# Kernel optimization log

Measured on AMD Instinct MI355X. Metric: run time of the kernel, lower is better.

## Reference

```python
import jax, jax.numpy as jnp
import numpy as np

DIM = 768; HEADS = 12; N_PH = 4; EXPERTS = 8; TOPK = 2; EXPERT_DIM = 3072; MEM_HEADS = 8; EPS = 1e-5


def phm_linear(x, A, S, b):
    # PHM linear: W = sum_i kron(A[i] (n,n), S[i] (out/n, in/n)) -> (out, in); y = x @ W.T + b
    out_f = A.shape[1] * S.shape[1]
    in_f = A.shape[2] * S.shape[2]
    W = jnp.einsum('iab,icd->acbd', A, S).reshape(out_f, in_f)
    return x @ W.T + b


def layernorm(x, g, b):
    m = x.mean(-1, keepdims=True)
    v = x.var(-1, keepdims=True)
    return (x - m) / jnp.sqrt(v + EPS) * g + b


def quantum_attn(x, A_qkv, S_qkv, b_qkv, A_p, S_p, b_p, w_sup, w_ent):
    B, N, C = x.shape
    hd = C // HEADS
    qkv = phm_linear(x, A_qkv, S_qkv, b_qkv).reshape(B, N, 3, HEADS, hd)
    qkv = qkv.transpose(2, 0, 3, 1, 4)  # (3,B,H,N,hd)
    q, k, v = qkv[0], qkv[1], qkv[2]
    attn = jnp.einsum('bhnd,bhmd->bhnm', q, k) * (hd ** -0.5)
    # superposition head-mixing: sup[:,i] = sum_j w_sup[i,j] * attn[:,j]
    sup = jnp.einsum('ij,bjnm->binm', w_sup, attn)
    # entanglement: ent[:,i] = tanh(sup[:,i] + sum_j w_ent[i,j] * sup[:,j])
    ent = jnp.tanh(sup + jnp.einsum('ij,bjnm->binm', w_ent, sup))
    a = jax.nn.softmax(ent, axis=-1)
    o = jnp.einsum('bhnm,bhmd->bnhd', a, v).reshape(B, N, C)
    return phm_linear(o, A_p, S_p, b_p)


def moe(x, rA, rS, rb, domain_routing, domain_id, eA, eS, eb, ndw, ndb):
    logits = phm_linear(x, rA, rS, rb) + domain_routing[domain_id]  # (B,N,E)
    topv, topi = jax.lax.top_k(logits, TOPK)
    w = jax.nn.softmax(topv, axis=-1)  # (B,N,K)
    onehot = (topi[..., None] == jnp.arange(EXPERTS)).astype(x.dtype)  # (B,N,K,E)
    gates = jnp.einsum('bnk,bnke->bne', w, onehot)  # combined top-k gate per expert

    def expert(Ae, Se, be, We, bne):
        h = jax.nn.gelu(phm_linear(x, Ae, Se, be), approximate=False)
        return h @ We.T + bne

    outs = jax.vmap(expert)(eA, eS, eb, ndw, ndb)  # (E,B,N,C)
    return jnp.einsum('bne,ebnc->bnc', gates, outs)


def mem_mha(x, mem, iw, ib, ow, ob):
    # standard MHA: queries from x (B,N,C), keys/values from memory bank (M,C) shared across batch
    B, N, C = x.shape
    dh = C // MEM_HEADS
    q = (x @ iw[:C].T + ib[:C]).reshape(B, N, MEM_HEADS, dh)
    k = (mem @ iw[C:2 * C].T + ib[C:2 * C]).reshape(-1, MEM_HEADS, dh)
    v = (mem @ iw[2 * C:].T + ib[2 * C:]).reshape(-1, MEM_HEADS, dh)
    a = jax.nn.softmax(jnp.einsum('bnhd,mhd->bhnm', q, k) * (dh ** -0.5), axis=-1)
    o = jnp.einsum('bhnm,mhd->bnhd', a, v).reshape(B, N, C)
    return o @ ow.T + ob


def fractal(x, mems, iw, ib, ow, ob, pw, pb):
    # recursive FractalMemoryBank unrolled for depth=3:
    # level l: a_l = proc_l(MHA_l(prev, mem_l)); return prev + deeper(a_l)
    a0 = mem_mha(x, mems[0], iw[0], ib[0], ow[0], ob[0]) @ pw[0].T + pb[0]
    a1 = mem_mha(a0, mems[1], iw[1], ib[1], ow[1], ob[1]) @ pw[1].T + pb[1]
    a2 = mem_mha(a1, mems[2], iw[2], ib[2], ow[2], ob[2]) @ pw[2].T + pb[2]
    return x + (a0 + (a1 + a2))


def _fwd(x, ln1_g, ln1_b, attn_qkv_A, attn_qkv_S, attn_qkv_b, attn_proj_A, attn_proj_S, attn_proj_b,
         w_sup, w_ent, ln2_g, ln2_b, router_A, router_S, router_b, domain_routing,
         exp_A, exp_S, exp_b, exp_nd_w, exp_nd_b, mem0, mem1, mem2,
         mha_in_w, mha_in_b, mha_out_w, mha_out_b, proc_w, proc_b, ln3_g, ln3_b, domain_id):
    attended = x + quantum_attn(layernorm(x, ln1_g, ln1_b), attn_qkv_A, attn_qkv_S, attn_qkv_b,
                                attn_proj_A, attn_proj_S, attn_proj_b, w_sup, w_ent)
    moe_out = moe(layernorm(attended, ln2_g, ln2_b), router_A, router_S, router_b,
                  domain_routing, domain_id, exp_A, exp_S, exp_b, exp_nd_w, exp_nd_b)
    eo = attended + moe_out
    mo = fractal(eo, (mem0, mem1, mem2), mha_in_w, mha_in_b, mha_out_w, mha_out_b, proc_w, proc_b)
    return layernorm(mo, ln3_g, ln3_b)


def setup_inputs():
    key = jax.random.key(0)
    ks = iter(jax.random.split(key, 40))

    def rn(shape, s=0.02):
        return s * jax.random.normal(next(ks), shape, dtype=jnp.float32)

    B, N = 4, 512
    ones = jnp.ones(DIM, jnp.float32)
    zeros = jnp.zeros(DIM, jnp.float32)
    return {
        'x': rn((B, N, DIM), 1.0),
        'ln1_g': ones, 'ln1_b': zeros, 'ln2_g': ones, 'ln2_b': zeros, 'ln3_g': ones, 'ln3_b': zeros,
        'attn_qkv_A': rn((N_PH, N_PH, N_PH), 0.3),
        'attn_qkv_S': rn((N_PH, 3 * DIM // N_PH, DIM // N_PH)),
        'attn_qkv_b': jnp.zeros(3 * DIM, jnp.float32),
        'attn_proj_A': rn((N_PH, N_PH, N_PH), 0.3),
        'attn_proj_S': rn((N_PH, DIM // N_PH, DIM // N_PH)),
        'attn_proj_b': zeros,
        'w_sup': rn((HEADS, HEADS), 0.2), 'w_ent': rn((HEADS, HEADS), 0.2),
        'router_A': rn((N_PH, N_PH, N_PH), 0.3),
        'router_S': rn((N_PH, EXPERTS // N_PH, DIM // N_PH)),
        'router_b': jnp.zeros(EXPERTS, jnp.float32),
        'domain_routing': rn((6, EXPERTS), 1.0),
        'exp_A': rn((EXPERTS, N_PH, N_PH, N_PH), 0.3),
        'exp_S': rn((EXPERTS, N_PH, EXPERT_DIM // N_PH, DIM // N_PH)),
        'exp_b': jnp.zeros((EXPERTS, EXPERT_DIM), jnp.float32),
        'exp_nd_w': rn((EXPERTS, DIM, EXPERT_DIM)),
        'exp_nd_b': jnp.zeros((EXPERTS, DIM), jnp.float32),
        'mem0': rn((64, DIM), 1.0), 'mem1': rn((128, DIM), 1.0), 'mem2': rn((256, DIM), 1.0),
        'mha_in_w': rn((3, 3 * DIM, DIM)), 'mha_in_b': jnp.zeros((3, 3 * DIM), jnp.float32),
        'mha_out_w': rn((3, DIM, DIM)), 'mha_out_b': jnp.zeros((3, DIM), jnp.float32),
        'proc_w': rn((3, DIM, DIM)), 'proc_b': jnp.zeros((3, DIM), jnp.float32),
        'domain_id': 2,
    }


def reference(x, ln1_g, ln1_b, ln2_g, ln2_b, ln3_g, ln3_b, attn_qkv_A, attn_qkv_S, attn_qkv_b,
              attn_proj_A, attn_proj_S, attn_proj_b, w_sup, w_ent, router_A, router_S, router_b,
              domain_routing, exp_A, exp_S, exp_b, exp_nd_w, exp_nd_b, mem0, mem1, mem2,
              mha_in_w, mha_in_b, mha_out_w, mha_out_b, proc_w, proc_b, domain_id):
    return _fwd(x, ln1_g, ln1_b, attn_qkv_A, attn_qkv_S, attn_qkv_b, attn_proj_A, attn_proj_S,
                attn_proj_b, w_sup, w_ent, ln2_g, ln2_b, router_A, router_S, router_b,
                domain_routing, exp_A, exp_S, exp_b, exp_nd_w, exp_nd_b, mem0, mem1, mem2,
                mha_in_w, mha_in_b, mha_out_w, mha_out_b, proc_w, proc_b, ln3_g, ln3_b, domain_id)
```

## Files before the change

kernel.cpp:

```cpp
#include <hip/hip_runtime.h>
#include <math.h>

#define DIM    768
#define NTOK   2048
#define NSEQ   512
#define NBATCH 4
#define NHEADS 12
#define HD     64
#define QKVC   2304
#define MHEADS 8
#define MHD    96
#define NEXP   8
#define EDIM   3072
#define DD     (DIM*DIM)

typedef unsigned short u16;
typedef __attribute__((ext_vector_type(8))) short short8;
typedef __attribute__((ext_vector_type(4))) float f32x4;

struct L3 { long a, b, c; };
struct I3 { int a, b, c; };
struct CJ { const float4* s[6]; ushort4* d[6]; int n4[6]; };

__device__ __forceinline__ float gelu_exact(float v){
    return 0.5f * v * (1.f + erff(v * 0.70710678118654752f));
}
__device__ __forceinline__ u16 f2bf(float f){
    unsigned int u = __builtin_bit_cast(unsigned int, f);
    unsigned int r = (u + 0x7FFFu + ((u >> 16) & 1u)) >> 16;
    return (u16)r;
}
__device__ __forceinline__ float bf2f(u16 b){
    unsigned int u = ((unsigned int)b) << 16;
    return __builtin_bit_cast(float, u);
}
__device__ __forceinline__ float fast_tanh(float s){
    return 1.f - 2.f/(__expf(2.f*s) + 1.f);
}
__device__ __forceinline__ void gll16(const u16* g, u16* l){
    __builtin_amdgcn_global_load_lds((const __attribute__((address_space(1))) void*)g,
                                     (__attribute__((address_space(3))) void*)l, 16, 0, 0);
}

template<int WM,int WN,int FR,int DB>
__device__ __forceinline__ void mgemm_core(
    const u16* __restrict__ Xb, int ldx, int rowBase, int rowLim,
    const u16* __restrict__ Wb, int ldw, int colBase, int colLim, int K,
    const float* __restrict__ bias,
    const float* __restrict__ res, int ldres,
    float* __restrict__ Cf, u16* __restrict__ Cb, int ldc,
    float scale, int act)
{
    constexpr int TM = 16*FR;
    constexpr int RM = WM*TM, RN = WN*TM, NT = WM*WN*64;
    constexpr int IA = (RM*8)/NT, IB = (RN*8)/NT;
    constexpr int NB = DB ? 2 : 1;
    __shared__ u16 As[NB][RM*64];
    __shared__ u16 Bs[NB][RN*64];
    int tid = threadIdx.x;
    int lane = tid & 63, w = tid >> 6;
    int wm = (w / WN) * TM, wn = (w % WN) * TM;
    const f32x4 zf = {0.f, 0.f, 0.f, 0.f};
    f32x4 acc[FR][FR];
    #pragma unroll
    for (int i=0;i<FR;i++)
        #pragma unroll
        for (int j=0;j<FR;j++) acc[i][j] = zf;

    const bool fullA = (rowBase + RM <= rowLim);
    const bool fullB = (colBase + RN <= colLim);
    const int nt = (K + 63) >> 6;
    int lr = lane & 15, lk = lane >> 4;

    auto stage = [&](int buf, int k0){
        const bool kfull = (k0 + 64 <= K);
        if (fullA && kfull) {
            #pragma unroll
            for (int it = 0; it < IA; ++it) {
                int idx = it*NT + tid;
                int r = idx >> 3, c = idx & 7;
                gll16(&Xb[(size_t)(rowBase + r)*ldx + k0 + ((c ^ (r & 7)) << 3)], &As[buf][(size_t)idx*8]);
            }
        } else {
            #pragma unroll
            for (int it = 0; it < IA; ++it) {
                int idx = it*NT + tid;
                int r = idx >> 3, c = idx & 7;
                int gr = rowBase + r;
                uint4 v = {0u,0u,0u,0u};
                if (gr < rowLim && (k0 + c*8) < K) v = *(const uint4*)&Xb[(size_t)gr*ldx + k0 + c*8];
                *(uint4*)&As[buf][r*64 + ((c ^ (r & 7)) * 8)] = v;
            }
        }
        if (fullB && kfull) {
            #pragma unroll
            for (int it = 0; it < IB; ++it) {
                int idx = it*NT + tid;
                int r = idx >> 3, c = idx & 7;
                gll16(&Wb[(size_t)(colBase + r)*ldw + k0 + ((c ^ (r & 7)) << 3)], &Bs[buf][(size_t)idx*8]);
            }
        } else {
            #pragma unroll
            for (int it = 0; it < IB; ++it) {
                int idx = it*NT + tid;
                int r = idx >> 3, c = idx & 7;
                int gc = colBase + r;
                uint4 v = {0u,0u,0u,0u};
                if (gc < colLim && (k0 + c*8) < K) v = *(const uint4*)&Wb[(size_t)gc*ldw + k0 + c*8];
                *(uint4*)&Bs[buf][r*64 + ((c ^ (r & 7)) * 8)] = v;
            }
        }
    };
    auto compute = [&](const u16* Ac, const u16* Bc){
        #pragma unroll
        for (int ks = 0; ks < 2; ++ks) {
            short8 af[FR], bfr[FR];
            #pragma unroll
            for (int mi=0; mi<FR; mi++){
                int row = wm + mi*16 + lr;
                int cidx = (ks*4 + lk) ^ (row & 7);
                af[mi] = *(const short8*)&Ac[row*64 + cidx*8];
            }
            #pragma unroll
            for (int ni=0; ni<FR; ni++){
                int col = wn + ni*16 + lr;
                int cidx = (ks*4 + lk) ^ (col & 7);
                bfr[ni] = *(const short8*)&Bc[col*64 + cidx*8];
            }
            #pragma unroll
            for (int mi=0; mi<FR; mi++)
                #pragma unroll
                for (int ni=0; ni<FR; ni++)
                    acc[mi][ni] = __builtin_amdgcn_mfma_f32_16x16x32_bf16(af[mi], bfr[ni], acc[mi][ni], 0, 0, 0);
        }
    };

    if (DB) {
        stage(0, 0);
        __syncthreads();
        for (int t = 0; t < nt; ++t) {
            if (t + 1 < nt) stage((t+1)&1, (t+1)*64);
            compute(As[t&1], Bs[t&1]);
            __syncthreads();
        }
    } else {
        for (int t = 0; t < nt; ++t) {
            stage(0, t*64);
            __syncthreads();
            compute(As[0], Bs[0]);
            __syncthreads();
        }
    }
    int lg = lane >> 4;
    #pragma unroll
    for (int mi=0; mi<FR; mi++){
        #pragma unroll
        for (int r=0; r<4; r++){
            int row = rowBase + wm + mi*16 + lg*4 + r;
            if (row >= rowLim) continue;
            #pragma unroll
            for (int ni=0; ni<FR; ni++){
                int col = colBase + wn + ni*16 + lr;
                if (col >= colLim) continue;
                float v = acc[mi][ni][r] * scale;
                if (bias) v += bias[col];
                if (act == 1) v = gelu_exact(v);
                if (Cb) Cb[(size_t)row*ldc + col] = f2bf(v);
                if (res) v += res[(size_t)row*ldres + col];
                if (Cf) Cf[(size_t)row*ldc + col] = v;
            }
        }
    }
}

template<int WM,int WN,int FR,int DB>
__global__ __launch_bounds__(WM*WN*64) void k_mgemm(
    const u16* __restrict__ X, int ldx, int M,
    const u16* __restrict__ W, int ldw, int N, int K,
    const float* __restrict__ bias, const float* __restrict__ res, int ldres,
    float* __restrict__ Cf, u16* __restrict__ Cb, int ldc, float scale, int act)
{
    constexpr int RM = WM*16*FR, RN = WN*16*FR;
    mgemm_core<WM,WN,FR,DB>(X, ldx, blockIdx.x*RM, M, W, ldw, blockIdx.y*RN, N, K,
                            bias, res, ldres, Cf, Cb, ldc, scale, act);
}

template<int WM,int WN,int FR,int DB>
__global__ __launch_bounds__(WM*WN*64) void k_mgemm_b3(
    const u16* __restrict__ X, L3 xo, int ldx, I3 Mv,
    const u16* __restrict__ W, L3 wo, int ldw, int N, int K,
    const float* __restrict__ bias, L3 bo,
    u16* __restrict__ Cb, L3 co, int ldc, float scale, int act)
{
    constexpr int RM = WM*16*FR, RN = WN*16*FR;
    int z = blockIdx.z;
    int M    = (z==0) ? Mv.a : (z==1) ? Mv.b : Mv.c;
    long xof = (z==0) ? xo.a : (z==1) ? xo.b : xo.c;
    long wof = (z==0) ? wo.a : (z==1) ? wo.b : wo.c;
    long bof = (z==0) ? bo.a : (z==1) ? bo.b : bo.c;
    long cof = (z==0) ? co.a : (z==1) ? co.b : co.c;
    if ((int)blockIdx.x * RM >= M) return;
    mgemm_core<WM,WN,FR,DB>(X + xof, ldx, blockIdx.x*RM, M, W + wof, ldw, blockIdx.y*RN, N, K,
                            bias ? bias + bof : nullptr, nullptr, 0, nullptr, Cb + cof, ldc, scale, act);
}

template<int WM,int WN,int FR,int DB>
__global__ __launch_bounds__(WM*WN*64) void k_mgemm_expert(
    const u16* __restrict__ X, int ldx,
    const u16* __restrict__ Wb, int ldw, long wStride,
    const float* __restrict__ biasB, int biasStride,
    const int* __restrict__ prefix, const int* __restrict__ cnt,
    float* __restrict__ Cf, u16* __restrict__ Cb, int ldc, int N, int K, int act)
{
    constexpr int RM = WM*16*FR, RN = WN*16*FR;
    int e = blockIdx.z;
    int n = cnt[e];
    if ((int)blockIdx.x * RM >= n) return;
    mgemm_core<WM,WN,FR,DB>(X, ldx, prefix[e] + blockIdx.x*RM, prefix[e] + n,
                            Wb + (size_t)e*wStride, ldw, blockIdx.y*RN, N, K,
                            biasB + (size_t)e*biasStride, nullptr, 0, Cf, Cb, ldc, 1.f, act);
}

template<int WM,int WN,int FR,int DB>
__global__ __launch_bounds__(WM*WN*64) void k_mgemm_qk(const u16* __restrict__ qkv, u16* __restrict__ attn)
{
    constexpr int RM = WM*16*FR, RN = WN*16*FR;
    int z = blockIdx.z, b = z / NHEADS, h = z % NHEADS;
    const u16* X = qkv + (size_t)b*NSEQ*QKVC + h*HD;
    const u16* W = qkv + (size_t)b*NSEQ*QKVC + DIM + h*HD;
    u16* C = attn + (size_t)z*NSEQ*NSEQ;
    mgemm_core<WM,WN,FR,DB>(X, QKVC, blockIdx.x*RM, NSEQ, W, QKVC, blockIdx.y*RN, NSEQ, HD,
                            nullptr, nullptr, 0, nullptr, C, NSEQ, 0.125f, 0);
}

template<int WM,int WN,int FR,int DB>
__global__ __launch_bounds__(WM*WN*64) void k_mgemm_pv(const u16* __restrict__ P, const u16* __restrict__ Vt, u16* __restrict__ o)
{
    constexpr int RM = WM*16*FR, RN = WN*16*FR;
    int z = blockIdx.z, b = z / NHEADS, h = z % NHEADS;
    const u16* X = P + (size_t)z*NSEQ*NSEQ;
    const u16* W = Vt + ((size_t)b*DIM + h*HD)*NSEQ;
    u16* C = o + (size_t)b*NSEQ*DIM + h*HD;
    mgemm_core<WM,WN,FR,DB>(X, NSEQ, blockIdx.x*RM, NSEQ, W, NSEQ, blockIdx.y*RN, HD, NSEQ,
                            nullptr, nullptr, 0, nullptr, C, DIM, 1.f, 0);
}

template<int WM,int WN,int FR,int DB>
__global__ __launch_bounds__(WM*WN*64) void k_gt(
    const u16* __restrict__ Wc, const u16* __restrict__ kvL, long kvStride,
    u16* __restrict__ Gt, long gtStride, I3 Mv)
{
    constexpr int RM = WM*16*FR, RN = WN*16*FR;
    int z = blockIdx.z, l = z >> 3, h = z & 7;
    int M = (l==0) ? Mv.a : (l==1) ? Mv.b : Mv.c;
    if ((int)blockIdx.y * RN >= M) return;
    mgemm_core<WM,WN,FR,DB>(Wc + (size_t)l*DD + h*MHD, DIM, blockIdx.x*RM, DIM,
                            kvL + (size_t)l*kvStride + DIM + h*MHD, 2*DIM, blockIdx.y*RN, M, MHD,
                            nullptr, nullptr, 0, nullptr,
                            Gt + (size_t)l*gtStride + (size_t)h*M, 8*M, 1.f, 0);
}

__global__ __launch_bounds__(256) void k_memqk_soft(
    const u16* __restrict__ q, const u16* __restrict__ kv, int ldk,
    u16* __restrict__ P, int M, float scale)
{
    constexpr int RM = 64, RN = 256, NT = 256, K = MHD;
    __shared__ u16 As[RM*64];
    __shared__ u16 Bs[RN*64];
    __shared__ float red0[RM][4];
    __shared__ float red1[RM][4];
    int h = blockIdx.y;
    int rowBase = blockIdx.x * RM;
    const u16* Xb = q + h*MHD;
    const u16* Wb = kv + h*MHD;
    int tid = threadIdx.x, lane = tid & 63, w = tid >> 6;
    int wn = w * 64;
    int lr = lane & 15, lk = lane >> 4;
    const f32x4 zf = {0.f,0.f,0.f,0.f};
    f32x4 acc[4][4];
    #pragma unroll
    for (int i=0;i<4;i++)
        #pragma unroll
        for (int j=0;j<4;j++) acc[i][j] = zf;

    for (int k0 = 0; k0 < K; k0 += 64) {
        const bool kfull = (k0 + 64 <= K);
        if (kfull) {
            #pragma unroll
            for (int it = 0; it < 2; ++it) {
                int idx = it*NT + tid;
                int r = idx >> 3, c = idx & 7;
                gll16(&Xb[(size_t)(rowBase + r)*DIM + k0 + ((c ^ (r & 7)) << 3)], &As[(size_t)idx*8]);
            }
        } else {
            #pragma unroll
            for (int it = 0; it < 2; ++it) {
                int idx = it*NT + tid;
                int r = idx >> 3, c = idx & 7;
                uint4 v = {0u,0u,0u,0u};
                if ((k0 + c*8) < K) v = *(const uint4*)&Xb[(size_t)(rowBase + r)*DIM + k0 + c*8];
                *(uint4*)&As[r*64 + ((c ^ (r & 7)) * 8)] = v;
            }
        }
        #pragma unroll
        for (int it = 0; it < 8; ++it) {
            int idx = it*NT + tid;
            int r = idx >> 3, c = idx & 7;
            uint4 v = {0u,0u,0u,0u};
            if (r < M && (k0 + c*8) < K) v = *(const uint4*)&Wb[(size_t)r*ldk + k0 + c*8];
            *(uint4*)&Bs[r*64 + ((c ^ (r & 7)) * 8)] = v;
        }
        __syncthreads();
        #pragma unroll
        for (int ks = 0; ks < 2; ++ks) {
            short8 af[4], bfr[4];
            #pragma unroll
            for (int mi=0; mi<4; mi++){
                int row = mi*16 + lr;
                int cidx = (ks*4 + lk) ^ (row & 7);
                af[mi] = *(const short8*)&As[row*64 + cidx*8];
            }
            #pragma unroll
            for (int ni=0; ni<4; ni++){
                int col = wn + ni*16 + lr;
                int cidx = (ks*4 + lk) ^ (col & 7);
                bfr[ni] = *(const short8*)&Bs[col*64 + cidx*8];
            }
            #pragma unroll
            for (int mi=0; mi<4; mi++)
                #pragma unroll
                for (int ni=0; ni<4; ni++)
                    acc[mi][ni] = __builtin_amdgcn_mfma_f32_16x16x32_bf16(af[mi], bfr[ni], acc[mi][ni], 0, 0, 0);
        }
        __syncthreads();
    }
    int lg = lane >> 4;
    float sc[4][4][4];
    float rmax[4][4];
    #pragma unroll
    for (int mi=0; mi<4; mi++){
        #pragma unroll
        for (int r=0; r<4; r++){
            float m = -1e30f;
            #pragma unroll
            for (int ni=0; ni<4; ni++){
                int col = wn + ni*16 + lr;
                float v = (col < M) ? acc[mi][ni][r]*scale : -1e30f;
                sc[mi][r][ni] = v;
                m = fmaxf(m, v);
            }
            m = fmaxf(m, __shfl_xor(m, 1));
            m = fmaxf(m, __shfl_xor(m, 2));
            m = fmaxf(m, __shfl_xor(m, 4));
            m = fmaxf(m, __shfl_xor(m, 8));
            rmax[mi][r] = m;
        }
    }
    if (lr == 0){
        #pragma unroll
        for (int mi=0; mi<4; mi++)
            #pragma unroll
            for (int r=0; r<4; r++) red0[mi*16 + lg*4 + r][w] = rmax[mi][r];
    }
    __syncthreads();
    float gmax[4][4], rsum[4][4];
    #pragma unroll
    for (int mi=0; mi<4; mi++){
        #pragma unroll
        for (int r=0; r<4; r++){
            int row = mi*16 + lg*4 + r;
            float g = fmaxf(fmaxf(red0[row][0], red0[row][1]), fmaxf(red0[row][2], red0[row][3]));
            gmax[mi][r] = g;
            float s = 0.f;
            #pragma unroll
            for (int ni=0; ni<4; ni++){
                int col = wn + ni*16 + lr;
                if (col < M) s += __expf(sc[mi][r][ni] - g);
            }
            s += __shfl_xor(s, 1);
            s += __shfl_xor(s, 2);
            s += __shfl_xor(s, 4);
            s += __shfl_xor(s, 8);
            rsum[mi][r] = s;
        }
    }
    if (lr == 0){
        #pragma unroll
        for (int mi=0; mi<4; mi++)
            #pragma unroll
            for (int r=0; r<4; r++) red1[mi*16 + lg*4 + r][w] = rsum[mi][r];
    }
    __syncthreads();
    #pragma unroll
    for (int mi=0; mi<4; mi++){
        #pragma unroll
        for (int r=0; r<4; r++){
            int row = mi*16 + lg*4 + r;
            float tot = red1[row][0] + red1[row][1] + red1[row][2] + red1[row][3];
            float inv = 1.f / tot;
            #pragma unroll
            for (int ni=0; ni<4; ni++){
                int col = wn + ni*16 + lr;
                if (col < M)
                    P[(((size_t)(rowBase + row))*MHEADS + h)*M + col] = f2bf(__expf(sc[mi][r][ni] - gmax[mi][r]) * inv);
            }
        }
    }
}

__global__ __launch_bounds__(256) void k_transw_b(const u16* __restrict__ src, u16* __restrict__ dst)
{
    int z = blockIdx.y;
    int idx = blockIdx.x*256 + threadIdx.x;
    int r = idx / DIM, c = idx % DIM;
    dst[(size_t)z*DD + (size_t)c*DIM + r] = src[(size_t)z*DD + (size_t)r*DIM + c];
}

__global__ __launch_bounds__(256) void k_phm4(
    const float* __restrict__ A, const float* __restrict__ S, void* __restrict__ W,
    int So, int Si, int inF, long Astride, long Sstride, long Wstride, int obf)
{
    int e = blockIdx.y;
    const float* Ae = A + (size_t)e*Astride;
    const float* Se = S + (size_t)e*Sstride;
    size_t idx = (size_t)blockIdx.x*256 + threadIdx.x;
    int inF4 = inF >> 2;
    size_t total = (size_t)(So*4) * inF4;
    if (idx >= total) return;
    int in4 = (int)(idx % inF4);
    int o   = (int)(idx / inF4);
    int a = o / So, c = o % So;
    int in0 = in4 * 4;
    int b = in0 / Si, d = in0 % Si;
    float4 acc = {0.f,0.f,0.f,0.f};
    #pragma unroll
    for (int i=0;i<4;i++){
        float av = Ae[i*16 + a*4 + b];
        float4 sv = *(const float4*)&Se[((size_t)i*So + c)*Si + d];
        acc.x = fmaf(av, sv.x, acc.x);
        acc.y = fmaf(av, sv.y, acc.y);
        acc.z = fmaf(av, sv.z, acc.z);
        acc.w = fmaf(av, sv.w, acc.w);
    }
    size_t oidx = (size_t)o*inF + in0;
    if (obf){
        ushort4 r; r.x=f2bf(acc.x); r.y=f2bf(acc.y); r.z=f2bf(acc.z); r.w=f2bf(acc.w);
        *(ushort4*)&((u16*)W)[(size_t)e*Wstride + oidx] = r;
    } else {
        *(float4*)&((float*)W)[(size_t)e*Wstride + oidx] = acc;
    }
}

__global__ __launch_bounds__(256) void k_cvt4(const float4* __restrict__ s, ushort4* __restrict__ d, int n4)
{
    for (int i = blockIdx.x*256 + threadIdx.x; i < n4; i += gridDim.x*256){
        float4 v = s[i];
        ushort4 o; o.x = f2bf(v.x); o.y = f2bf(v.y); o.z = f2bf(v.z); o.w = f2bf(v.w);
        d[i] = o;
    }
}
__global__ __launch_bounds__(256) void k_cvt_multi(CJ J)
{
    int z = blockIdx.y;
    const float4* s = J.s[z]; ushort4* d = J.d[z]; int n4 = J.n4[z];
    for (int i = blockIdx.x*256 + threadIdx.x; i < n4; i += gridDim.x*256){
        float4 v = s[i];
        ushort4 o; o.x = f2bf(v.x); o.y = f2bf(v.y); o.z = f2bf(v.z); o.w = f2bf(v.w);
        d[i] = o;
    }
}

__global__ __launch_bounds__(256) void k_bc(const float* __restrict__ pw, const float* __restrict__ outb,
                                            const float* __restrict__ pb, float* __restrict__ bc)
{
    int l = blockIdx.y;
    int i = blockIdx.x*4 + (threadIdx.x >> 6);
    int lane = threadIdx.x & 63;
    const float* pr = pw + ((size_t)l*DIM + i)*DIM;
    const float* ob = outb + (size_t)l*DIM;
    float s = 0.f;
    for (int j = lane; j < DIM; j += 64) s = fmaf(pr[j], ob[j], s);
    for (int off=32; off; off>>=1) s += __shfl_xor(s, off);
    if (lane == 0) bc[(size_t)l*DIM + i] = s + pb[(size_t)l*DIM + i];
}

__global__ __launch_bounds__(256) void k_ln(const float* __restrict__ x, const float* __restrict__ g,
                                            const float* __restrict__ b,
                                            float* __restrict__ yf, u16* __restrict__ yb)
{
    int row = blockIdx.x, tid = threadIdx.x;
    const float* xr = x + (size_t)row * DIM;
    float v0 = xr[tid], v1 = xr[tid+256], v2 = xr[tid+512];
    float s = v0+v1+v2;
    float ss = v0*v0 + v1*v1 + v2*v2;
    for (int off=32; off; off>>=1){ s += __shfl_xor(s,off); ss += __shfl_xor(ss,off); }
    __shared__ float sa[4], sb[4];
    int wid = tid >> 6;
    if ((tid & 63) == 0){ sa[wid]=s; sb[wid]=ss; }
    __syncthreads();
    s  = sa[0]+sa[1]+sa[2]+sa[3];
    ss = sb[0]+sb[1]+sb[2]+sb[3];
    float mean = s * (1.f/DIM);
    float var  = ss * (1.f/DIM) - mean*mean;
    float rstd = rsqrtf(var + 1e-5f);
    float o0 = (v0-mean)*rstd*g[tid]     + b[tid];
    float o1 = (v1-mean)*rstd*g[tid+256] + b[tid+256];
    float o2 = (v2-mean)*rstd*g[tid+512] + b[tid+512];
    if (yf){ float* yr = yf + (size_t)row*DIM; yr[tid]=o0; yr[tid+256]=o1; yr[tid+512]=o2; }
    if (yb){ u16* yr = yb + (size_t)row*DIM; yr[tid]=f2bf(o0); yr[tid+256]=f2bf(o1); yr[tid+512]=f2bf(o2); }
}

__global__ __launch_bounds__(256) void k_supsoft(
    const u16* __restrict__ attn, u16* __restrict__ P,
    const float* __restrict__ wsup, const float* __restrict__ went)
{
    __shared__ float S[NHEADS][NSEQ];
    __shared__ float ws[144], we[144];
    int bn = blockIdx.x;
    int b = bn >> 9, n = bn & 511;
    int tid = threadIdx.x;
    if (tid < 144){ ws[tid] = wsup[tid]; we[tid] = went[tid]; }
    size_t base = ((size_t)b*NHEADS*NSEQ + n)*NSEQ;
    #pragma unroll
    for (int it=0; it<3; ++it){
        int idx = it*256 + tid;
        int j = idx >> 6, m8 = (idx & 63) * 8;
        uint4 v = *(const uint4*)&attn[base + (size_t)j*NSEQ*NSEQ + m8];
        S[j][m8+0] = bf2f((u16)(v.x & 0xFFFFu)); S[j][m8+1] = bf2f((u16)(v.x >> 16));
        S[j][m8+2] = bf2f((u16)(v.y & 0xFFFFu)); S[j][m8+3] = bf2f((u16)(v.y >> 16));
        S[j][m8+4] = bf2f((u16)(v.z & 0xFFFFu)); S[j][m8+5] = bf2f((u16)(v.z >> 16));
        S[j][m8+6] = bf2f((u16)(v.w & 0xFFFFu)); S[j][m8+7] = bf2f((u16)(v.w >> 16));
    }
    __syncthreads();
    #pragma unroll
    for (int half=0; half<2; ++half){
        int m = tid + half*256;
        float av[12], sup[12];
        #pragma unroll
        for (int j=0;j<12;j++) av[j] = S[j][m];
        #pragma unroll
        for (int i=0;i<12;i++){
            float s = 0.f;
            #pragma unroll
            for (int j=0;j<12;j++) s = fmaf(ws[i*12+j], av[j], s);
            sup[i] = s;
        }
        #pragma unroll
        for (int i=0;i<12;i++){
            float s = sup[i];
            #pragma unroll
            for (int j=0;j<12;j++) s = fmaf(we[i*12+j], sup[j], s);
            av[i] = fast_tanh(s);
        }
        #pragma unroll
        for (int i=0;i<12;i++) S[i][m] = av[i];
    }
    __syncthreads();
    int lane = tid & 63, wv = tid >> 6;
    #pragma unroll
    for (int jj=0; jj<3; ++jj){
        int j = wv*3 + jj;
        float v[8], mx = -1e30f;
        #pragma unroll
        for (int k=0;k<8;k++){ v[k] = S[j][lane + 64*k]; mx = fmaxf(mx, v[k]); }
        for (int off=32; off; off>>=1) mx = fmaxf(mx, __shfl_xor(mx, off));
        float sum = 0.f;
        #pragma unroll
        for (int k=0;k<8;k++){ v[k] = __expf(v[k]-mx); sum += v[k]; }
        for (int off=32; off; off>>=1) sum += __shfl_xor(sum, off);
        float inv = 1.f/sum;
        #pragma unroll
        for (int k=0;k<8;k++) P[base + (size_t)j*NSEQ*NSEQ + lane + 64*k] = f2bf(v[k]*inv);
    }
}

__global__ __launch_bounds__(256) void k_transv(const u16* __restrict__ qkv, u16* __restrict__ Vt)
{
    __shared__ u16 L[64][65];
    int mt = blockIdx.x*64, dt = blockIdx.y*64, b = blockIdx.z;
    int tid = threadIdx.x;
    #pragma unroll
    for (int it=0; it<16; ++it){
        int idx = it*256 + tid;
        int mm = idx >> 6, dd = idx & 63;
        L[mm][dd] = qkv[((size_t)b*NSEQ + mt + mm)*QKVC + 1536 + dt + dd];
    }
    __syncthreads();
    #pragma unroll
    for (int it=0; it<16; ++it){
        int idx = it*256 + tid;
        int dd = idx >> 6, mm = idx & 63;
        Vt[((size_t)b*DIM + dt + dd)*NSEQ + mt + mm] = L[mm][dd];
    }
}

__global__ __launch_bounds__(256) void k_route(
    const u16* __restrict__ ln2, const float* __restrict__ Wr,
    const float* __restrict__ rb, const float* __restrict__ dr,
    const int* __restrict__ did, int* __restrict__ topi, float* __restrict__ topw, int* __restrict__ cnt)
{
    int t = blockIdx.x, tid = threadIdx.x;
    const u16* xr = ln2 + (size_t)t*DIM;
    float a[8] = {};
    #pragma unroll
    for (int ii=0; ii<3; ii++){
        int i = tid + ii*256;
        float xv = bf2f(xr[i]);
        #pragma unroll
        for (int e=0;e<8;e++) a[e] = fmaf(xv, Wr[e*DIM + i], a[e]);
    }
    #pragma unroll
    for (int e=0;e<8;e++)
        for (int off=32; off; off>>=1) a[e] += __shfl_xor(a[e], off);
    __shared__ float sred[4][8];
    int wid = tid >> 6;
    if ((tid & 63) == 0){
        #pragma unroll
        for (int e=0;e<8;e++) sred[wid][e] = a[e];
    }
    __syncthreads();
    if (tid == 0){
        int d = did[0];
        float lg[8];
        #pragma unroll
        for (int e=0;e<8;e++) lg[e] = sred[0][e]+sred[1][e]+sred[2][e]+sred[3][e] + rb[e] + dr[d*8+e];
        int i1 = 0; float v1 = lg[0];
        #pragma unroll
        for (int e=1;e<8;e++) if (lg[e] > v1){ v1 = lg[e]; i1 = e; }
        int i2 = -1; float v2 = -1e30f;
        #pragma unroll
        for (int e=0;e<8;e++) if (e != i1 && lg[e] > v2){ v2 = lg[e]; i2 = e; }
        float e2 = __expf(v2 - v1);
        float inv = 1.f / (1.f + e2);
        topi[2*t] = i1; topi[2*t+1] = i2;
        topw[2*t] = inv; topw[2*t+1] = e2 * inv;
        atomicAdd(&cnt[i1], 1); atomicAdd(&cnt[i2], 1);
    }
}

__global__ void k_zero(int* p, int n){ int i = threadIdx.x; if (i < n) p[i] = 0; }

__global__ void k_prefix(const int* __restrict__ cnt, int* __restrict__ prefix){
    if (threadIdx.x == 0){ int s=0; for (int e=0;e<8;e++){ prefix[e]=s; s+=cnt[e]; } }
}

__global__ __launch_bounds__(256) void k_assign(
    const int* __restrict__ topi, const int* __restrict__ prefix,
    int* __restrict__ cnt2, int* __restrict__ rowof, int* __restrict__ tokof)
{
    int t = blockIdx.x*256 + threadIdx.x;
    if (t >= NTOK) return;
    #pragma unroll
    for (int k=0;k<2;k++){
        int e = topi[2*t+k];
        int slot = atomicAdd(&cnt2[e], 1);
        int row = prefix[e] + slot;
        rowof[2*t+k] = row;
        tokof[row] = t;
    }
}

__global__ __launch_bounds__(256) void k_gather(const u16* __restrict__ src, const int* __restrict__ tokof, u16* __restrict__ dst)
{
    int i = blockIdx.x*256 + threadIdx.x;
    int row = i / 96, c = (i % 96) * 8;
    *(uint4*)&dst[(size_t)row*DIM + c] = *(const uint4*)&src[(size_t)tokof[row]*DIM + c];
}

__global__ __launch_bounds__(256) void k_combine(
    const float* __restrict__ att, const float* __restrict__ outg,
    const int* __restrict__ rowof, const float* __restrict__ topw,
    float* __restrict__ eo, u16* __restrict__ eob)
{
    size_t i = (size_t)blockIdx.x*256 + threadIdx.x;
    int t = (int)(i / DIM), c = (int)(i % DIM);
    int r0 = rowof[2*t], r1 = rowof[2*t+1];
    float v = att[i] + topw[2*t]*outg[(size_t)r0*DIM+c] + topw[2*t+1]*outg[(size_t)r1*DIM+c];
    eo[i] = v;
    eob[i] = f2bf(v);
}

extern "C" void kernel_launch(void* const* d_in, const int* in_sizes, int n_in,
                              void* d_out, int out_size, void* d_ws, size_t ws_size,
                              hipStream_t stream)
{
    const float* x     = (const float*)d_in[0];
    const float* ln1g  = (const float*)d_in[1];
    const float* ln1b  = (const float*)d_in[2];
    const float* ln2g  = (const float*)d_in[3];
    const float* ln2b  = (const float*)d_in[4];
    const float* ln3g  = (const float*)d_in[5];
    const float* ln3b  = (const float*)d_in[6];
    const float* qkvA  = (const float*)d_in[7];
    const float* qkvS  = (const float*)d_in[8];
    const float* qkvb  = (const float*)d_in[9];
    const float* projA = (const float*)d_in[10];
    const float* projS = (const float*)d_in[11];
    const float* projb = (const float*)d_in[12];
    const float* wsup  = (const float*)d_in[13];
    const float* went  = (const float*)d_in[14];
    const float* rA    = (const float*)d_in[15];
    const float* rS    = (const float*)d_in[16];
    const float* rb    = (const float*)d_in[17];
    const float* dr    = (const float*)d_in[18];
    const float* eA    = (const float*)d_in[19];
    const float* eS    = (const float*)d_in[20];
    const float* eb    = (const float*)d_in[21];
    const float* ndw   = (const float*)d_in[22];
    const float* ndb   = (const float*)d_in[23];
    const float* mem0  = (const float*)d_in[24];
    const float* mem1  = (const float*)d_in[25];
    const float* mem2  = (const float*)d_in[26];
    const float* inw   = (const float*)d_in[27];
    const float* inb   = (const float*)d_in[28];
    const float* outw  = (const float*)d_in[29];
    const float* outb  = (const float*)d_in[30];
    const float* pw    = (const float*)d_in[31];
    const float* pb    = (const float*)d_in[32];
    const int*   did   = (const int*)d_in[33];

    float* f = (float*)d_ws;
    size_t off = 0;
    auto alloc = [&](size_t n){ float* p = f + off; off += (n + 3) & ~(size_t)3; return p; };
    auto allocb = [&](size_t n){ return (u16*)alloc((n + 1) / 2); };

    float* attnd  = alloc((size_t)NTOK*DIM);
    float* eo     = alloc((size_t)NTOK*DIM);
    float* accum  = alloc((size_t)NTOK*DIM);
    float* attnb  = alloc((size_t)48*NSEQ*NSEQ);
    float* Wrout  = alloc((size_t)NEXP*DIM);
    float* topw   = alloc((size_t)2*NTOK);
    float* bcb    = alloc((size_t)3*DIM);
    int* ip = (int*)alloc((size_t)6*NTOK + 64);
    int* topi   = ip;            ip += 2*NTOK;
    int* rowof  = ip;            ip += 2*NTOK;
    int* tokof  = ip;            ip += 2*NTOK;
    int* cnt    = ip;            ip += 8;
    int* cnt2   = ip;            ip += 8;
    int* prefix = ip;            ip += 8;

    u16*   scores = (u16*)attnb;
    float* outg   = attnb;
    u16*   ndw_bf = (u16*)(attnb + (size_t)3146240);

    u16* Wqkv_bf  = allocb((size_t)QKVC*DIM);
    u16* Wproj_bf = allocb((size_t)DD);
    u16* Wexp_bf  = allocb((size_t)NEXP*EDIM*DIM);
    u16* inw_bf   = allocb((size_t)3*QKVC*DIM);
    u16* outw_bf  = allocb((size_t)3*DD);
    u16* pw_bf    = allocb((size_t)3*DD);
    u16* Wc_bf    = allocb((size_t)3*DD);
    u16* wT3_bf   = allocb((size_t)3*DD);
    u16* mem_bf   = allocb((size_t)448*DIM);
    u16* qkv_bf   = allocb((size_t)NTOK*QKVC);
    u16* Vt_bf    = allocb((size_t)NBATCH*DIM*NSEQ);
    u16* P_bf     = allocb((size_t)48*NSEQ*NSEQ);
    u16* lnx_bf   = allocb((size_t)NTOK*DIM);
    u16* o_bf     = allocb((size_t)NTOK*DIM);
    u16* inx_bf   = allocb((size_t)NTOK*DIM);
    u16* kvL_bf   = allocb((size_t)3*256*2*DIM);
    u16* Gt_bf    = allocb((size_t)3*768*2048);
    u16* Xg_bf    = qkv_bf;
    u16* hidden_bf= P_bf;
    u16* Pm_bf    = P_bf;
    u16* qm_bf    = o_bf;

    float* outf = (float*)d_out;
    dim3 T256(256), T64(64);
    I3 Ms3 = {64, 128, 256};

    k_zero<<<1, 32, 0, stream>>>(cnt, 16);
    k_ln<<<NTOK, T256, 0, stream>>>(x, ln1g, ln1b, nullptr, lnx_bf);
    k_phm4<<<dim3(1728,1), T256, 0, stream>>>(qkvA, qkvS, Wqkv_bf, 576, 192, DIM, 0,0,0, 1);
    k_phm4<<<dim3(576,1),  T256, 0, stream>>>(projA, projS, Wproj_bf, 192, 192, DIM, 0,0,0, 1);
    k_phm4<<<dim3(6,1),    T256, 0, stream>>>(rA, rS, Wrout, 2, 192, DIM, 0,0,0, 0);
    k_phm4<<<dim3(2304,NEXP), T256, 0, stream>>>(eA, eS, Wexp_bf, 768, 192, DIM,
                                                 64L, (long)4*768*192, (long)EDIM*DIM, 1);
    {
        CJ J;
        J.s[0]=(const float4*)inw;  J.d[0]=(ushort4*)inw_bf;  J.n4[0]=3*QKVC*DIM/4;
        J.s[1]=(const float4*)outw; J.d[1]=(ushort4*)outw_bf; J.n4[1]=3*DD/4;
        J.s[2]=(const float4*)pw;   J.d[2]=(ushort4*)pw_bf;   J.n4[2]=3*DD/4;
        J.s[3]=(const float4*)mem0; J.d[3]=(ushort4*)mem_bf;              J.n4[3]=64*DIM/4;
        J.s[4]=(const float4*)mem1; J.d[4]=(ushort4*)(mem_bf + 64*DIM);   J.n4[4]=128*DIM/4;
        J.s[5]=(const float4*)mem2; J.d[5]=(ushort4*)(mem_bf + 192*DIM);  J.n4[5]=256*DIM/4;
        k_cvt_multi<<<dim3(1024, 6), T256, 0, stream>>>(J);
    }
    k_bc<<<dim3(DIM/4, 3), T256, 0, stream>>>(pw, outb, pb, bcb);
    k_transw_b<<<dim3(DD/256, 3), T256, 0, stream>>>(outw_bf, wT3_bf);
    {
        L3 dd3 = {0, DD, 2*DD}, z3 = {0,0,0};
        I3 m768 = {DIM, DIM, DIM};
        k_mgemm_b3<2,2,2,1><<<dim3(12,12,3), T256, 0, stream>>>(pw_bf, dd3, DIM, m768,
                                                                wT3_bf, dd3, DIM, DIM, DIM,
                                                                nullptr, z3, Wc_bf, dd3, DIM, 1.f, 0);
    }
    {
        L3 xo = {0, 64L*DIM, 192L*DIM};
        L3 wo = {(long)DD, (long)QKVC*DIM + DD, 2L*QKVC*DIM + DD};
        L3 bo = {(long)DIM, (long)QKVC + DIM, 2L*QKVC + DIM};
        L3 co = {0, 256L*2*DIM, 2*256L*2*DIM};
        k_mgemm_b3<1,1,2,1><<<dim3(8,48,3), T64, 0, stream>>>(mem_bf, xo, DIM, Ms3,
                                                              inw_bf, wo, DIM, 2*DIM, DIM,
                                                              inb, bo, kvL_bf, co, 2*DIM, 1.f, 0);
    }
    k_gt<2,2,2,1><<<dim3(12,4,24), T256, 0, stream>>>(Wc_bf, kvL_bf, 256L*2*DIM, Gt_bf, 768L*2048, Ms3);

    k_mgemm<2,2,2,1><<<dim3(32,36), T256, 0, stream>>>(lnx_bf, DIM, NTOK, Wqkv_bf, DIM, QKVC, DIM,
                                                       qkvb, nullptr, 0, nullptr, qkv_bf, QKVC, 1.f, 0);
    k_transv<<<dim3(8,12,NBATCH), T256, 0, stream>>>(qkv_bf, Vt_bf);
    k_mgemm_qk<2,2,2,1><<<dim3(8,8,48), T256, 0, stream>>>(qkv_bf, scores);
    k_supsoft<<<dim3(NTOK), T256, 0, stream>>>(scores, P_bf, wsup, went);
    k_cvt4<<<4096, T256, 0, stream>>>((const float4*)ndw, (ushort4*)ndw_bf, NEXP*DIM*EDIM/4);
    k_mgemm_pv<1,1,2,1><<<dim3(16,2,48), T64, 0, stream>>>(P_bf, Vt_bf, o_bf);
    k_mgemm<2,2,1,1><<<dim3(64,24), T256, 0, stream>>>(o_bf, DIM, NTOK, Wproj_bf, DIM, DIM, DIM,
                                                       projb, x, DIM, attnd, nullptr, DIM, 1.f, 0);
    k_ln<<<NTOK, T256, 0, stream>>>(attnd, ln2g, ln2b, nullptr, lnx_bf);
    k_route<<<NTOK, T256, 0, stream>>>(lnx_bf, Wrout, rb, dr, did, topi, topw, cnt);
    k_prefix<<<1, 1, 0, stream>>>(cnt, prefix);
    k_assign<<<8, T256, 0, stream>>>(topi, prefix, cnt2, rowof, tokof);
    k_gather<<<dim3(1536), T256, 0, stream>>>(lnx_bf, tokof, Xg_bf);
    k_mgemm_expert<2,2,2,1><<<dim3(32,48,NEXP), T256, 0, stream>>>(Xg_bf, DIM, Wexp_bf, DIM, (long)EDIM*DIM,
                                                                   eb, EDIM, prefix, cnt,
                                                                   nullptr, hidden_bf, EDIM, EDIM, DIM, 1);
    k_mgemm_expert<2,2,1,1><<<dim3(64,24,NEXP), T256, 0, stream>>>(hidden_bf, EDIM, ndw_bf, EDIM, (long)DIM*EDIM,
                                                                   ndb, DIM, prefix, cnt,
                                                                   outg, nullptr, DIM, DIM, EDIM, 0);
    k_combine<<<dim3(6144), T256, 0, stream>>>(attnd, outg, rowof, topw, eo, inx_bf);
    int Ms[3] = {64, 128, 256};
    for (int l=0; l<3; ++l){
        const u16* iwl = inw_bf + (size_t)l*QKVC*DIM;
        int M = Ms[l];
        k_mgemm<2,2,1,1><<<dim3(64,24), T256, 0, stream>>>(inx_bf, DIM, NTOK, iwl, DIM, DIM, DIM,
                                                           inb + (size_t)l*QKVC, nullptr, 0, nullptr, qm_bf, DIM, 1.f, 0);
        k_memqk_soft<<<dim3(NTOK/64, MHEADS), T256, 0, stream>>>(qm_bf, kvL_bf + (size_t)l*256*2*DIM, 2*DIM,
                                                                 Pm_bf, M, 0.10206207261596577f);
        k_mgemm<2,2,1,1><<<dim3(64,24), T256, 0, stream>>>(Pm_bf, 8*M, NTOK, Gt_bf + (size_t)l*768*2048, 8*M, DIM, 8*M,
                                                           bcb + (size_t)l*DIM, (l==0 ? eo : accum), DIM,
                                                           accum, inx_bf, DIM, 1.f, 0);
    }
    k_ln<<<NTOK, T256, 0, stream>>>(accum, ln3g, ln3b, outf, nullptr);
}
```

Before: 595.3 us.

## Flatten expert GEMM grids with 64-aligned per-expert row padding

Pads each expert's row segment to a multiple of 64 and launches the expert GEMMs over a flat row grid, so each block finds its expert from the prefix array. This replaces the per-expert z-dimension grid, where most blocks exit early, with one sized to the actual padded token count. Blocks should also no longer straddle an expert boundary. The bf16 conversion of the down-projection weights moves to a dedicated buffer earlier in the stream, and Xg gets its own padded buffer with tokof zeroed. The cost is extra memory and possibly wasted padded-row compute in the gather.

```diff
diff --git a/kernel.cpp b/kernel.cpp
--- a/kernel.cpp
+++ b/kernel.cpp
@@ -13,6 +13,7 @@
 #define NEXP   8
 #define EDIM   3072
 #define DD     (DIM*DIM)
+#define PADROWS 4608
 
 typedef unsigned short u16;
 typedef __attribute__((ext_vector_type(8))) short short8;
@@ -205,7 +206,7 @@
 }
 
 template<int WM,int WN,int FR,int DB>
-__global__ __launch_bounds__(WM*WN*64) void k_mgemm_expert(
+__global__ __launch_bounds__(WM*WN*64) void k_mgemm_expert_flat(
     const u16* __restrict__ X, int ldx,
     const u16* __restrict__ Wb, int ldw, long wStride,
     const float* __restrict__ biasB, int biasStride,
@@ -213,10 +214,14 @@
     float* __restrict__ Cf, u16* __restrict__ Cb, int ldc, int N, int K, int act)
 {
     constexpr int RM = WM*16*FR, RN = WN*16*FR;
-    int e = blockIdx.z;
-    int n = cnt[e];
-    if ((int)blockIdx.x * RM >= n) return;
-    mgemm_core<WM,WN,FR,DB>(X, ldx, prefix[e] + blockIdx.x*RM, prefix[e] + n,
+    int rowBase = (int)blockIdx.x * RM;
+    if (rowBase >= prefix[8]) return;
+    int e = 0;
+    #pragma unroll
+    for (int i=0;i<7;i++) if (rowBase >= prefix[i+1]) e = i+1;
+    int rowLim = prefix[e] + cnt[e];
+    if (rowBase >= rowLim) return;
+    mgemm_core<WM,WN,FR,DB>(X, ldx, rowBase, rowLim,
                             Wb + (size_t)e*wStride, ldw, blockIdx.y*RN, N, K,
                             biasB + (size_t)e*biasStride, nullptr, 0, Cf, Cb, ldc, 1.f, act);
 }
@@ -638,10 +643,14 @@
     }
 }
 
-__global__ void k_zero(int* p, int n){ int i = threadIdx.x; if (i < n) p[i] = 0; }
+__global__ void k_zero(int* p, int n){ int i = blockIdx.x*256 + threadIdx.x; if (i < n) p[i] = 0; }
 
 __global__ void k_prefix(const int* __restrict__ cnt, int* __restrict__ prefix){
-    if (threadIdx.x == 0){ int s=0; for (int e=0;e<8;e++){ prefix[e]=s; s+=cnt[e]; } }
+    if (threadIdx.x == 0){
+        int s = 0;
+        for (int e=0;e<8;e++){ prefix[e] = s; s += (cnt[e] + 63) & ~63; }
+        prefix[8] = s;
+    }
 }
 
 __global__ __launch_bounds__(256) void k_assign(
@@ -731,21 +740,22 @@
     float* Wrout  = alloc((size_t)NEXP*DIM);
     float* topw   = alloc((size_t)2*NTOK);
     float* bcb    = alloc((size_t)3*DIM);
-    int* ip = (int*)alloc((size_t)6*NTOK + 64);
+    int* ip = (int*)alloc((size_t)4*NTOK + PADROWS + 64);
     int* topi   = ip;            ip += 2*NTOK;
     int* rowof  = ip;            ip += 2*NTOK;
-    int* tokof  = ip;            ip += 2*NTOK;
+    int* tokof  = ip;            ip += PADROWS;
     int* cnt    = ip;            ip += 8;
     int* cnt2   = ip;            ip += 8;
-    int* prefix = ip;            ip += 8;
+    int* prefix = ip;            ip += 16;
 
     u16*   scores = (u16*)attnb;
     float* outg   = attnb;
-    u16*   ndw_bf = (u16*)(attnb + (size_t)3146240);
+    u16*   ndw_bf = (u16*)(attnb + (size_t)3538944);
 
     u16* Wqkv_bf  = allocb((size_t)QKVC*DIM);
     u16* Wproj_bf = allocb((size_t)DD);
     u16* Wexp_bf  = allocb((size_t)NEXP*EDIM*DIM);
+    u16* ndw_bf2  = allocb((size_t)NEXP*DIM*EDIM);
     u16* inw_bf   = allocb((size_t)3*QKVC*DIM);
     u16* outw_bf  = allocb((size_t)3*DD);
     u16* pw_bf    = allocb((size_t)3*DD);
@@ -754,13 +764,13 @@
     u16* mem_bf   = allocb((size_t)448*DIM);
     u16* qkv_bf   = allocb((size_t)NTOK*QKVC);
     u16* Vt_bf    = allocb((size_t)NBATCH*DIM*NSEQ);
-    u16* P_bf     = allocb((size_t)48*NSEQ*NSEQ);
+    u16* P_bf     = allocb((size_t)PADROWS*EDIM);
     u16* lnx_bf   = allocb((size_t)NTOK*DIM);
     u16* o_bf     = allocb((size_t)NTOK*DIM);
     u16* inx_bf   = allocb((size_t)NTOK*DIM);
+    u16* Xg_bf    = allocb((size_t)PADROWS*DIM);
     u16* kvL_bf   = allocb((size_t)3*256*2*DIM);
     u16* Gt_bf    = allocb((size_t)3*768*2048);
-    u16* Xg_bf    = qkv_bf;
     u16* hidden_bf= P_bf;
     u16* Pm_bf    = P_bf;
     u16* qm_bf    = o_bf;
@@ -770,6 +780,7 @@
     I3 Ms3 = {64, 128, 256};
 
     k_zero<<<1, 32, 0, stream>>>(cnt, 16);
+    k_zero<<<(PADROWS+255)/256, T256, 0, stream>>>(tokof, PADROWS);
     k_ln<<<NTOK, T256, 0, stream>>>(x, ln1g, ln1b, nullptr, lnx_bf);
     k_phm4<<<dim3(1728,1), T256, 0, stream>>>(qkvA, qkvS, Wqkv_bf, 576, 192, DIM, 0,0,0, 1);
     k_phm4<<<dim3(576,1),  T256, 0, stream>>>(projA, projS, Wproj_bf, 192, 192, DIM, 0,0,0, 1);
@@ -805,13 +816,13 @@
                                                               inb, bo, kvL_bf, co, 2*DIM, 1.f, 0);
     }
     k_gt<2,2,2,1><<<dim3(12,4,24), T256, 0, stream>>>(Wc_bf, kvL_bf, 256L*2*DIM, Gt_bf, 768L*2048, Ms3);
+    k_cvt4<<<4096, T256, 0, stream>>>((const float4*)ndw, (ushort4*)ndw_bf2, NEXP*DIM*EDIM/4);
 
     k_mgemm<2,2,2,1><<<dim3(32,36), T256, 0, stream>>>(lnx_bf, DIM, NTOK, Wqkv_bf, DIM, QKVC, DIM,
                                                        qkvb, nullptr, 0, nullptr, qkv_bf, QKVC, 1.f, 0);
     k_transv<<<dim3(8,12,NBATCH), T256, 0, stream>>>(qkv_bf, Vt_bf);
     k_mgemm_qk<2,2,2,1><<<dim3(8,8,48), T256, 0, stream>>>(qkv_bf, scores);
     k_supsoft<<<dim3(NTOK), T256, 0, stream>>>(scores, P_bf, wsup, went);
-    k_cvt4<<<4096, T256, 0, stream>>>((const float4*)ndw, (ushort4*)ndw_bf, NEXP*DIM*EDIM/4);
     k_mgemm_pv<1,1,2,1><<<dim3(16,2,48), T64, 0, stream>>>(P_bf, Vt_bf, o_bf);
     k_mgemm<2,2,1,1><<<dim3(64,24), T256, 0, stream>>>(o_bf, DIM, NTOK, Wproj_bf, DIM, DIM, DIM,
                                                        projb, x, DIM, attnd, nullptr, DIM, 1.f, 0);
@@ -819,13 +830,13 @@
     k_route<<<NTOK, T256, 0, stream>>>(lnx_bf, Wrout, rb, dr, did, topi, topw, cnt);
     k_prefix<<<1, 1, 0, stream>>>(cnt, prefix);
     k_assign<<<8, T256, 0, stream>>>(topi, prefix, cnt2, rowof, tokof);
-    k_gather<<<dim3(1536), T256, 0, stream>>>(lnx_bf, tokof, Xg_bf);
-    k_mgemm_expert<2,2,2,1><<<dim3(32,48,NEXP), T256, 0, stream>>>(Xg_bf, DIM, Wexp_bf, DIM, (long)EDIM*DIM,
-                                                                   eb, EDIM, prefix, cnt,
-                                                                   nullptr, hidden_bf, EDIM, EDIM, DIM, 1);
-    k_mgemm_expert<2,2,1,1><<<dim3(64,24,NEXP), T256, 0, stream>>>(hidden_bf, EDIM, ndw_bf, EDIM, (long)DIM*EDIM,
-                                                                   ndb, DIM, prefix, cnt,
-                                                                   outg, nullptr, DIM, DIM, EDIM, 0);
+    k_gather<<<dim3(PADROWS*96/256), T256, 0, stream>>>(lnx_bf, tokof, Xg_bf);
+    k_mgemm_expert_flat<2,2,2,1><<<dim3(PADROWS/64, 48), T256, 0, stream>>>(Xg_bf, DIM, Wexp_bf, DIM, (long)EDIM*DIM,
+                                                                            eb, EDIM, prefix, cnt,
+                                                                            nullptr, hidden_bf, EDIM, EDIM, DIM, 1);
+    k_mgemm_expert_flat<2,2,1,1><<<dim3(PADROWS/32, 24), T256, 0, stream>>>(hidden_bf, EDIM, ndw_bf2, EDIM, (long)DIM*EDIM,
+                                                                            ndb, DIM, prefix, cnt,
+                                                                            outg, nullptr, DIM, DIM, EDIM, 0);
     k_combine<<<dim3(6144), T256, 0, stream>>>(attnd, outg, rowof, topw, eo, inx_bf);
     int Ms[3] = {64, 128, 256};
     for (int l=0; l<3; ++l){
```

Measured after the change: 594.7 us. About the same (-0.1%).
